# Kernel optimization log

Measured on AMD Instinct MI355X. Metric: run time of the kernel, lower is better.

Reference implementation:

```python
import jax, jax.numpy as jnp
import numpy as np

N_ENTITIES = 4096
FEATURE_DIM = 512
CELLS = 39
PAIRS = 8192


def setup_inputs() -> dict:
    key = jax.random.key(0)
    k_emb, k_idx, k_wg, k_wl = jax.random.split(key, 4)
    embedding = jax.random.normal(k_emb, (N_ENTITIES, FEATURE_DIM), dtype=jnp.float32)
    index = jax.random.randint(k_idx, (CELLS, PAIRS, 2), 0, N_ENTITIES, dtype=jnp.int32)
    # kaiming_uniform-style scale for the global bilinear weight
    bound_g = np.sqrt(6.0 / FEATURE_DIM)
    weights_global = jax.random.uniform(k_wg, (FEATURE_DIM, FEATURE_DIM), minval=-bound_g, maxval=bound_g, dtype=jnp.float32)
    # per-cell diagonal scaling vectors (original stores them as [d,1] params)
    weights_local = jax.random.uniform(k_wl, (CELLS, FEATURE_DIM), minval=-bound_g, maxval=bound_g, dtype=jnp.float32)
    return {"embedding": embedding, "index": index,
            "weights_global": weights_global, "weights_local": weights_local}


def reference(embedding, index, weights_global, weights_local):
    # Original per-cell math: einsum('bn,nm,mj,jk,bk->b', A, diag(wl), W, diag(wl), B)
    # diag(wl) @ ... is just elementwise scaling of the gathered embeddings, so:
    #   out[c,p] = sum_{n,k} (A[c,p,n]*wl[c,n]) * W[n,k] * (B[c,p,k]*wl[c,k])
    wl = weights_local[:, None, :]                      # [C,1,d]
    A = embedding[index[..., 0]] * wl                   # [C,P,d]
    B = embedding[index[..., 1]] * wl                   # [C,P,d]
    return jnp.einsum('cpn,nk,cpk->cp', A, weights_global, B)  # [C,P]
```

## Files before the change

### kernel.cpp

```cpp
#include <hip/hip_runtime.h>
#include <stdint.h>

#define NE 4096
#define FD 512
#define NCELLS 39
#define NPAIRS 8192

typedef __attribute__((ext_vector_type(8))) short short8;
typedef __attribute__((ext_vector_type(8))) unsigned short ushort8;
typedef __attribute__((ext_vector_type(4))) float f32x4;
typedef __attribute__((ext_vector_type(4))) unsigned int uint4v;

__device__ __forceinline__ unsigned short f2bf(float f) {
  union { float f; uint32_t u; } v; v.f = f;
  uint32_t u = v.u;
  return (unsigned short)((u + 0x7fffu + ((u >> 16) & 1u)) >> 16);
}
__device__ __forceinline__ float bf2f(unsigned short b) {
  return __uint_as_float(((uint32_t)b) << 16);
}

__device__ __forceinline__ void async16(const void* g, void* l) {
  __builtin_amdgcn_global_load_lds((const __attribute__((address_space(1))) void*)g,
                                   (__attribute__((address_space(3))) void*)l, 16, 0, 0);
}

__global__ __launch_bounds__(256) void conv_e(const float* __restrict__ E,
                                              unsigned short* __restrict__ Ebf) {
  const int i = blockIdx.x * 256 + threadIdx.x;
  const float4 v = ((const float4*)E)[i];
  ushort4 o;
  o.x = f2bf(v.x); o.y = f2bf(v.y); o.z = f2bf(v.z); o.w = f2bf(v.w);
  ((ushort4*)Ebf)[i] = o;
}

__global__ __launch_bounds__(256) void prep_w(const float* __restrict__ W,
                                              const float* __restrict__ wl,
                                              unsigned short* __restrict__ Wt,
                                              int c0) {
  __shared__ float tile[32][33];
  const int ci = blockIdx.z;
  const int tn = blockIdx.x * 32, tk = blockIdx.y * 32;
  const int tx = threadIdx.x & 31, ty = threadIdx.x >> 5;
  const float* wlr = wl + (size_t)(c0 + ci) * FD;
#pragma unroll
  for (int i = 0; i < 4; i++) {
    int n = tn + ty + i * 8;
    tile[ty + i * 8][tx] = W[(size_t)n * FD + tk + tx] * wlr[n];
  }
  __syncthreads();
  unsigned short* dst = Wt + (size_t)ci * FD * FD;
#pragma unroll
  for (int i = 0; i < 4; i++) {
    int kout = tk + ty + i * 8;
    dst[(size_t)kout * FD + tn + tx] = f2bf(tile[tx][ty + i * 8] * wlr[kout]);
  }
}

__global__ __launch_bounds__(256) void gemm_k(const unsigned short* __restrict__ Ebf,
                                              const unsigned short* __restrict__ Wt,
                                              unsigned short* __restrict__ U) {
  __shared__ unsigned short As[128 * 32];
  __shared__ unsigned short Bs[128 * 32];
  const int t = threadIdx.x;
  const int ci = blockIdx.z;
  const unsigned short* Ag = Ebf + (size_t)blockIdx.x * 128 * FD;
  const unsigned short* Bg = Wt + (size_t)ci * FD * FD + (size_t)blockIdx.y * 128 * FD;

  f32x4 acc[4][4];
#pragma unroll
  for (int i = 0; i < 4; i++)
#pragma unroll
    for (int j = 0; j < 4; j++) acc[i][j] = (f32x4){0.f, 0.f, 0.f, 0.f};

  const int wave = t >> 6, lane = t & 63;
  const int wm = (wave & 1) * 64, wn = (wave >> 1) * 64;
  const int lr = lane & 15, lq = lane >> 4;
  const int idx0 = t, idx1 = 256 + t;
  const int r0 = idx0 >> 2, cb0 = (idx0 & 3) * 8;
  const int r1 = idx1 >> 2, cb1 = (idx1 & 3) * 8;

  for (int k0 = 0; k0 < FD; k0 += 32) {
    async16(Ag + (size_t)r0 * FD + k0 + cb0, &As[idx0 * 8]);
    async16(Ag + (size_t)r1 * FD + k0 + cb1, &As[idx1 * 8]);
    async16(Bg + (size_t)r0 * FD + k0 + cb0, &Bs[idx0 * 8]);
    async16(Bg + (size_t)r1 * FD + k0 + cb1, &Bs[idx1 * 8]);
    __syncthreads();
    short8 af[4], bq[4];
#pragma unroll
    for (int mi = 0; mi < 4; mi++) af[mi] = *(const short8*)&As[(wm + mi * 16 + lr) * 32 + lq * 8];
#pragma unroll
    for (int ni = 0; ni < 4; ni++) bq[ni] = *(const short8*)&Bs[(wn + ni * 16 + lr) * 32 + lq * 8];
#pragma unroll
    for (int mi = 0; mi < 4; mi++)
#pragma unroll
      for (int ni = 0; ni < 4; ni++)
        acc[mi][ni] = __builtin_amdgcn_mfma_f32_16x16x32_bf16(af[mi], bq[ni], acc[mi][ni], 0, 0, 0);
    __syncthreads();
  }

  unsigned short* Up = U + (size_t)ci * NE * FD;
#pragma unroll
  for (int mi = 0; mi < 4; mi++) {
    int mbase = blockIdx.x * 128 + wm + mi * 16 + lq * 4;
#pragma unroll
    for (int ni = 0; ni < 4; ni++) {
      int n = blockIdx.y * 128 + wn + ni * 16 + lr;
#pragma unroll
      for (int r = 0; r < 4; r++) {
        Up[(size_t)(mbase + r) * FD + n] = f2bf(acc[mi][ni][r]);
      }
    }
  }
}

__global__ __launch_bounds__(256) void dot_k(const unsigned short* __restrict__ U,
                                             const unsigned short* __restrict__ Ebf,
                                             const int* __restrict__ index,
                                             float* __restrict__ out,
                                             int c0) {
  const int ci = blockIdx.y;
  const int c = c0 + ci;
  const int wave = threadIdx.x >> 6, lane = threadIdx.x & 63;
  const unsigned short* Uc = U + (size_t)ci * NE * FD;
  const size_t cp = (size_t)c * NPAIRS;
  const int2* idx2 = (const int2*)index + cp;
  float* op = out + cp;
  const int pbase = (blockIdx.x * 4 + wave) * 32;

  for (int batch = 0; batch < 4; batch++) {
    const int pb = pbase + batch * 8;
    int2 id[8];
#pragma unroll
    for (int b = 0; b < 8; b++) id[b] = idx2[pb + b];
    uint4v uv[8], ev[8];
#pragma unroll
    for (int b = 0; b < 8; b++) {
      uv[b] = __builtin_nontemporal_load((const uint4v*)(Uc + (size_t)id[b].x * FD + lane * 8));
      ev[b] = *(const uint4v*)(Ebf + (size_t)id[b].y * FD + lane * 8);
    }
#pragma unroll
    for (int b = 0; b < 8; b++) {
      const ushort8 u = *(const ushort8*)&uv[b];
      const ushort8 e = *(const ushort8*)&ev[b];
      float s = 0.f;
#pragma unroll
      for (int q = 0; q < 8; q++) s += bf2f(u[q]) * bf2f(e[q]);
      s += __shfl_xor(s, 1, 64);
      s += __shfl_xor(s, 2, 64);
      s += __shfl_xor(s, 4, 64);
      s += __shfl_xor(s, 8, 64);
      s += __shfl_xor(s, 16, 64);
      s += __shfl_xor(s, 32, 64);
      if (lane == b) op[pb + b] = s;
    }
  }
}

__global__ __launch_bounds__(256) void naive_k(const float* __restrict__ emb,
                                               const int* __restrict__ index,
                                               const float* __restrict__ W,
                                               const float* __restrict__ wl,
                                               float* __restrict__ out) {
  __shared__ float bs[FD];
  __shared__ float red[256];
  const int c = blockIdx.y, p = blockIdx.x;
  const int i0 = index[((size_t)c * NPAIRS + p) * 2];
  const int i1 = index[((size_t)c * NPAIRS + p) * 2 + 1];
  const float* wlc = wl + (size_t)c * FD;
  for (int k = threadIdx.x; k < FD; k += 256) bs[k] = emb[(size_t)i1 * FD + k] * wlc[k];
  __syncthreads();
  float s = 0.f;
  for (int n = threadIdx.x; n < FD; n += 256) {
    const float* wr = W + (size_t)n * FD;
    float tacc = 0.f;
    for (int k = 0; k < FD; k++) tacc += wr[k] * bs[k];
    s += tacc * emb[(size_t)i0 * FD + n] * wlc[n];
  }
  red[threadIdx.x] = s;
  __syncthreads();
  for (int st = 128; st > 0; st >>= 1) {
    if (threadIdx.x < st) red[threadIdx.x] += red[threadIdx.x + st];
    __syncthreads();
  }
  if (threadIdx.x == 0) out[(size_t)c * NPAIRS + p] = red[0];
}

extern "C" void kernel_launch(void* const* d_in, const int* in_sizes, int n_in,
                              void* d_out, int out_size, void* d_ws, size_t ws_size,
                              hipStream_t stream) {
  const float* emb = (const float*)d_in[0];
  const int* index = (const int*)d_in[1];
  const float* Wg = (const float*)d_in[2];
  const float* wl = (const float*)d_in[3];
  float* out = (float*)d_out;

  const size_t ebytes = (size_t)NE * FD * 2;
  const size_t wtcell = (size_t)FD * FD * 2;
  const size_t ucell = (size_t)NE * FD * 2;
  size_t avail = ws_size > ebytes ? ws_size - ebytes : 0;
  int G = (int)(avail / (wtcell + ucell));
  if (G > NCELLS) G = NCELLS;

  if (G < 1) {
    naive_k<<<dim3(NPAIRS, NCELLS), 256, 0, stream>>>(emb, index, Wg, wl, out);
    return;
  }

  unsigned short* Ebf = (unsigned short*)d_ws;
  unsigned short* Wt = (unsigned short*)((char*)d_ws + ebytes);
  unsigned short* U = (unsigned short*)((char*)d_ws + ebytes + (size_t)G * wtcell);

  conv_e<<<dim3((NE * FD / 4) / 256), 256, 0, stream>>>(emb, Ebf);
  for (int c0 = 0; c0 < NCELLS; c0 += G) {
    int g = (NCELLS - c0 < G) ? (NCELLS - c0) : G;
    prep_w<<<dim3(FD / 32, FD / 32, g), 256, 0, stream>>>(Wg, wl, Wt, c0);
    gemm_k<<<dim3(NE / 128, FD / 128, g), 256, 0, stream>>>(Ebf, Wt, U);
    dot_k<<<dim3(NPAIRS / 128, g), 256, 0, stream>>>(U, Ebf, index, out, c0);
  }
}
```

Before: 248.7 us.

## Rewrite bilinear GEMM as 256x256 double-buffered swizzled pipeline; streamline dot reduction

The per-cell GEMM now uses 256x256 output tiles with 512 threads and a 1D grid remapped across XCDs. It keeps a double-buffered LDS ring with an XOR-swizzled layout, and an interleaved schedule overlaps async global-to-LDS loads with MFMA phases, with explicit waitcnt and barrier placement and raised issue priority around the MFMAs. This targets the low reuse, small K-step and fully serialized load/compute of the old 128x128 kernel. In dot_k, the eight per-pair dot products are reduced together with a transpose-style butterfly to cut shuffle count, and the U gather no longer uses nontemporal loads so rows can stay in cache. The cost is about 128KB of LDS per block, which limits occupancy, plus fragile hand-scheduled synchronization.

```diff
diff --git a/kernel.cpp b/kernel.cpp
--- a/kernel.cpp
+++ b/kernel.cpp
@@ -5,6 +5,7 @@
 #define FD 512
 #define NCELLS 39
 #define NPAIRS 8192
+#define NT (FD / 64)
 
 typedef __attribute__((ext_vector_type(8))) short short8;
 typedef __attribute__((ext_vector_type(8))) unsigned short ushort8;
@@ -57,61 +58,146 @@
   }
 }
 
-__global__ __launch_bounds__(256) void gemm_k(const unsigned short* __restrict__ Ebf,
-                                              const unsigned short* __restrict__ Wt,
-                                              unsigned short* __restrict__ U) {
-  __shared__ unsigned short As[128 * 32];
-  __shared__ unsigned short Bs[128 * 32];
+__global__ __launch_bounds__(512, 2) void gemm_k(const unsigned short* __restrict__ Ebf,
+                                                 const unsigned short* __restrict__ Wt,
+                                                 unsigned short* __restrict__ U) {
+  __shared__ unsigned short lds[2][2][2][128 * 64];
   const int t = threadIdx.x;
-  const int ci = blockIdx.z;
-  const unsigned short* Ag = Ebf + (size_t)blockIdx.x * 128 * FD;
-  const unsigned short* Bg = Wt + (size_t)ci * FD * FD + (size_t)blockIdx.y * 128 * FD;
-
-  f32x4 acc[4][4];
-#pragma unroll
-  for (int i = 0; i < 4; i++)
+  const int nwg = gridDim.x;
+  const int id = blockIdx.x;
+  const int fid = (id & 7) * (nwg >> 3) + (id >> 3);
+  const int bx = fid & 15;
+  const int by = (fid >> 4) & 1;
+  const int ci = fid >> 5;
+
+  const unsigned short* Ag = Ebf + (size_t)bx * 256 * FD;
+  const unsigned short* Bg = Wt + (size_t)ci * FD * FD + (size_t)by * 256 * FD;
+
+  const int wave = t >> 6, lane = t & 63;
+  const int wm = wave >> 2, wn = wave & 3;
+  const int lr = lane & 15, lq = lane >> 4;
+
+  const int pg0 = t, pg1 = 512 + t;
+  const int sr0 = pg0 >> 3, sg0 = pg0 & 7;
+  const int sr1 = pg1 >> 3, sg1 = pg1 & 7;
+  const int soff0 = sr0 * FD + ((sg0 ^ (sr0 & 7)) << 3);
+  const int soff1 = sr1 * FD + ((sg1 ^ (sr1 & 7)) << 3);
+  const int loff0 = pg0 * 8, loff1 = pg1 * 8;
+
+  const int swz0 = (lq ^ (lr & 7)) << 3;
+  const int swz1 = ((4 + lq) ^ (lr & 7)) << 3;
+
+#define STAGE(OP, HALF, KT, GBASE)                                                \
+  do {                                                                            \
+    const int bi_ = (KT) & 1;                       \
+    const int kt_ = (KT) < NT ? (KT) : (NT - 1);       \
+    const unsigned short* gb_ = (GBASE) + (size_t)(HALF) * (128 * FD) + kt_ * 64; \
+    unsigned short* d_ = &lds[bi_][OP][HALF][0];                                  \
+    async16(gb_ + soff0, d_ + loff0);                                             \
+    async16(gb_ + soff1, d_ + loff1);                                             \
+  } while (0)
+
+  short8 a[8], b01[4], b23[4];
+  f32x4 acc[8][4];
+#pragma unroll
+  for (int i = 0; i < 8; i++)
 #pragma unroll
     for (int j = 0; j < 4; j++) acc[i][j] = (f32x4){0.f, 0.f, 0.f, 0.f};
 
-  const int wave = t >> 6, lane = t & 63;
-  const int wm = (wave & 1) * 64, wn = (wave >> 1) * 64;
-  const int lr = lane & 15, lq = lane >> 4;
-  const int idx0 = t, idx1 = 256 + t;
-  const int r0 = idx0 >> 2, cb0 = (idx0 & 3) * 8;
-  const int r1 = idx1 >> 2, cb1 = (idx1 & 3) * 8;
-
-  for (int k0 = 0; k0 < FD; k0 += 32) {
-    async16(Ag + (size_t)r0 * FD + k0 + cb0, &As[idx0 * 8]);
-    async16(Ag + (size_t)r1 * FD + k0 + cb1, &As[idx1 * 8]);
-    async16(Bg + (size_t)r0 * FD + k0 + cb0, &Bs[idx0 * 8]);
-    async16(Bg + (size_t)r1 * FD + k0 + cb1, &Bs[idx1 * 8]);
-    __syncthreads();
-    short8 af[4], bq[4];
-#pragma unroll
-    for (int mi = 0; mi < 4; mi++) af[mi] = *(const short8*)&As[(wm + mi * 16 + lr) * 32 + lq * 8];
-#pragma unroll
-    for (int ni = 0; ni < 4; ni++) bq[ni] = *(const short8*)&Bs[(wn + ni * 16 + lr) * 32 + lq * 8];
-#pragma unroll
-    for (int mi = 0; mi < 4; mi++)
-#pragma unroll
-      for (int ni = 0; ni < 4; ni++)
-        acc[mi][ni] = __builtin_amdgcn_mfma_f32_16x16x32_bf16(af[mi], bq[ni], acc[mi][ni], 0, 0, 0);
-    __syncthreads();
+#define LDA(BUF, MSET)                                                  \
+  do {                                                                  \
+    const unsigned short* p_ = &lds[BUF][0][wm][0];                     \
+    _Pragma("unroll") for (int mi_ = 0; mi_ < 4; ++mi_) {               \
+      const int row_ = (MSET) * 64 + mi_ * 16 + lr;                     \
+      a[mi_ * 2 + 0] = *(const short8*)&p_[row_ * 64 + swz0];           \
+      a[mi_ * 2 + 1] = *(const short8*)&p_[row_ * 64 + swz1];           \
+    }                                                                   \
+  } while (0)
+
+#define LDB(BUF, NSET, DST)                                             \
+  do {                                                                  \
+    const unsigned short* p_ = &lds[BUF][1][wn >> 1][0];                \
+    _Pragma("unroll") for (int ni_ = 0; ni_ < 2; ++ni_) {               \
+      const int row_ = (wn & 1) * 64 + ((NSET) * 2 + ni_) * 16 + lr;    \
+      (DST)[ni_ * 2 + 0] = *(const short8*)&p_[row_ * 64 + swz0];       \
+      (DST)[ni_ * 2 + 1] = *(const short8*)&p_[row_ * 64 + swz1];       \
+    }                                                                   \
+  } while (0)
+
+#define MMA(MSET, NSET, B)                                                               \
+  do {                                                                                   \
+    __builtin_amdgcn_s_setprio(1);                                                       \
+    _Pragma("unroll") for (int mi_ = 0; mi_ < 4; ++mi_)                                  \
+    _Pragma("unroll") for (int ni_ = 0; ni_ < 2; ++ni_)                                  \
+    _Pragma("unroll") for (int s_ = 0; s_ < 2; ++s_)                                     \
+      acc[(MSET) * 4 + mi_][(NSET) * 2 + ni_] = __builtin_amdgcn_mfma_f32_16x16x32_bf16( \
+          a[mi_ * 2 + s_], (B)[ni_ * 2 + s_],                                            \
+          acc[(MSET) * 4 + mi_][(NSET) * 2 + ni_], 0, 0, 0);                             \
+    __builtin_amdgcn_s_setprio(0);                                                       \
+  } while (0)
+
+#define SYNC_LG()                                        \
+  do {                                                   \
+    __builtin_amdgcn_s_barrier();                        \
+    asm volatile("s_waitcnt lgkmcnt(0)" ::: "memory");   \
+  } while (0)
+
+  STAGE(1, 0, 0, Bg); STAGE(0, 0, 0, Ag); STAGE(1, 1, 0, Bg); STAGE(0, 1, 0, Ag);
+  STAGE(1, 0, 1, Bg); STAGE(0, 0, 1, Ag);
+  asm volatile("s_waitcnt vmcnt(4)" ::: "memory");
+  __builtin_amdgcn_s_barrier();
+
+  for (int it = 0; it < NT / 2; ++it) {
+    const int k1 = 2 * it + 1, k2 = 2 * it + 2, k3 = 2 * it + 3;
+    LDA(0, 0); LDB(0, 0, b01);
+    STAGE(1, 1, k1, Bg);
+    SYNC_LG(); MMA(0, 0, b01); __builtin_amdgcn_s_barrier();
+    LDB(0, 1, b23);
+    STAGE(0, 1, k1, Ag);
+    SYNC_LG(); MMA(0, 1, b23); __builtin_amdgcn_s_barrier();
+    LDA(0, 1);
+    STAGE(1, 0, k2, Bg);
+    SYNC_LG(); MMA(1, 1, b23); __builtin_amdgcn_s_barrier();
+    STAGE(0, 0, k2, Ag);
+    __builtin_amdgcn_s_barrier();
+    MMA(1, 0, b01);
+    asm volatile("s_waitcnt vmcnt(4)" ::: "memory");
+    __builtin_amdgcn_s_barrier();
+    LDA(1, 0); LDB(1, 0, b01);
+    STAGE(1, 1, k2, Bg);
+    SYNC_LG(); MMA(0, 0, b01); __builtin_amdgcn_s_barrier();
+    LDB(1, 1, b23);
+    STAGE(0, 1, k2, Ag);
+    SYNC_LG(); MMA(0, 1, b23); __builtin_amdgcn_s_barrier();
+    LDA(1, 1);
+    STAGE(1, 0, k3, Bg);
+    SYNC_LG(); MMA(1, 1, b23); __builtin_amdgcn_s_barrier();
+    STAGE(0, 0, k3, Ag);
+    __builtin_amdgcn_s_barrier();
+    MMA(1, 0, b01);
+    asm volatile("s_waitcnt vmcnt(4)" ::: "memory");
+    __builtin_amdgcn_s_barrier();
   }
 
   unsigned short* Up = U + (size_t)ci * NE * FD;
-#pragma unroll
-  for (int mi = 0; mi < 4; mi++) {
-    int mbase = blockIdx.x * 128 + wm + mi * 16 + lq * 4;
-#pragma unroll
-    for (int ni = 0; ni < 4; ni++) {
-      int n = blockIdx.y * 128 + wn + ni * 16 + lr;
-#pragma unroll
-      for (int r = 0; r < 4; r++) {
+  const int mrow0 = bx * 256 + wm * 128;
+  const int ncol0 = by * 256 + wn * 64;
+#pragma unroll
+  for (int mi = 0; mi < 8; ++mi) {
+    const int mbase = mrow0 + mi * 16 + lq * 4;
+#pragma unroll
+    for (int ni = 0; ni < 4; ++ni) {
+      const int n = ncol0 + ni * 16 + lr;
+#pragma unroll
+      for (int r = 0; r < 4; ++r)
         Up[(size_t)(mbase + r) * FD + n] = f2bf(acc[mi][ni][r]);
-      }
-    }
-  }
+    }
+  }
+#undef STAGE
+#undef LDA
+#undef LDB
+#undef MMA
+#undef SYNC_LG
 }
 
 __global__ __launch_bounds__(256) void dot_k(const unsigned short* __restrict__ U,
@@ -128,6 +214,8 @@
   float* op = out + cp;
   const int pbase = (blockIdx.x * 4 + wave) * 32;
 
+  const int b1 = lane & 1, b2 = (lane >> 1) & 1, b4 = (lane >> 2) & 1;
+
   for (int batch = 0; batch < 4; batch++) {
     const int pb = pbase + batch * 8;
     int2 id[8];
@@ -136,9 +224,10 @@
     uint4v uv[8], ev[8];
 #pragma unroll
     for (int b = 0; b < 8; b++) {
-      uv[b] = __builtin_nontemporal_load((const uint4v*)(Uc + (size_t)id[b].x * FD + lane * 8));
+      uv[b] = *(const uint4v*)(Uc + (size_t)id[b].x * FD + lane * 8);
       ev[b] = *(const uint4v*)(Ebf + (size_t)id[b].y * FD + lane * 8);
     }
+    float v[8];
 #pragma unroll
     for (int b = 0; b < 8; b++) {
       const ushort8 u = *(const ushort8*)&uv[b];
@@ -146,14 +235,32 @@
       float s = 0.f;
 #pragma unroll
       for (int q = 0; q < 8; q++) s += bf2f(u[q]) * bf2f(e[q]);
-      s += __shfl_xor(s, 1, 64);
-      s += __shfl_xor(s, 2, 64);
-      s += __shfl_xor(s, 4, 64);
-      s += __shfl_xor(s, 8, 64);
-      s += __shfl_xor(s, 16, 64);
-      s += __shfl_xor(s, 32, 64);
-      if (lane == b) op[pb + b] = s;
-    }
+      v[b] = s;
+    }
+    float w[4];
+#pragma unroll
+    for (int q = 0; q < 4; q++) {
+      const float keep = b1 ? v[2 * q + 1] : v[2 * q];
+      const float send = b1 ? v[2 * q] : v[2 * q + 1];
+      w[q] = keep + __shfl_xor(send, 1, 64);
+    }
+    float u2[2];
+#pragma unroll
+    for (int q = 0; q < 2; q++) {
+      const float keep = b2 ? w[2 * q + 1] : w[2 * q];
+      const float send = b2 ? w[2 * q] : w[2 * q + 1];
+      u2[q] = keep + __shfl_xor(send, 2, 64);
+    }
+    float f;
+    {
+      const float keep = b4 ? u2[1] : u2[0];
+      const float send = b4 ? u2[0] : u2[1];
+      f = keep + __shfl_xor(send, 4, 64);
+    }
+    f += __shfl_xor(f, 8, 64);
+    f += __shfl_xor(f, 16, 64);
+    f += __shfl_xor(f, 32, 64);
+    if (lane < 8) op[pb + lane] = f;
   }
 }
 
@@ -215,7 +322,7 @@
   for (int c0 = 0; c0 < NCELLS; c0 += G) {
     int g = (NCELLS - c0 < G) ? (NCELLS - c0) : G;
     prep_w<<<dim3(FD / 32, FD / 32, g), 256, 0, stream>>>(Wg, wl, Wt, c0);
-    gemm_k<<<dim3(NE / 128, FD / 128, g), 256, 0, stream>>>(Ebf, Wt, U);
+    gemm_k<<<dim3(32 * g), 512, 0, stream>>>(Ebf, Wt, U);
     dot_k<<<dim3(NPAIRS / 128, g), 256, 0, stream>>>(U, Ebf, index, out, c0);
   }
 }
```

Measured after the change: 243.2 us. 2.2% less time.
